# Optimization experiments

Measured on AMD Instinct MI355X. Metric: run time of the kernel, lower is better.

Reference implementation:

```python
import jax, jax.numpy as jnp
import numpy as np

EPS = 1e-5

def _layer_norm(x, gamma, beta):
    mu = jnp.mean(x, axis=-1, keepdims=True)
    var = jnp.mean(jnp.square(x - mu), axis=-1, keepdims=True)
    return (x - mu) * jax.lax.rsqrt(var + EPS) * gamma + beta

def setup_inputs() -> dict:
    key = jax.random.key(0)
    ks = jax.random.split(key, 6)
    B, D, H = 8192, 1024, 1024
    x = jax.random.normal(ks[0], (B, D), dtype=jnp.float32)
    h0 = jax.random.normal(ks[1], (B, H), dtype=jnp.float32)
    c0 = jax.random.normal(ks[2], (B, H), dtype=jnp.float32)
    # learned params (orthogonal init approximated by scaled normal for reference purposes)
    weight_h = jax.random.normal(ks[3], (H, 4 * H), dtype=jnp.float32) / np.sqrt(H)
    weight_x = jax.random.normal(ks[4], (D, 4 * H), dtype=jnp.float32) / np.sqrt(D)
    bias = jnp.zeros((4 * H,), dtype=jnp.float32).at[:H].set(1.0)  # forget-gate bias init to 1
    ln1_g = jnp.ones((4 * H,), jnp.float32); ln1_b = jnp.zeros((4 * H,), jnp.float32)
    ln2_g = jnp.ones((4 * H,), jnp.float32); ln2_b = jnp.zeros((4 * H,), jnp.float32)
    ln3_g = jnp.ones((H,), jnp.float32); ln3_b = jnp.zeros((H,), jnp.float32)
    return {"x": x, "h0": h0, "c0": c0, "weight_h": weight_h, "weight_x": weight_x,
            "bias": bias, "ln1_g": ln1_g, "ln1_b": ln1_b, "ln2_g": ln2_g, "ln2_b": ln2_b,
            "ln3_g": ln3_g, "ln3_b": ln3_b}

def reference(x, h0, c0, weight_h, weight_x, bias, ln1_g, ln1_b, ln2_g, ln2_b, ln3_g, ln3_b):
    # gates: [B, 4H] = LN(h0 @ Wh) + LN(x @ Wx) + bias
    gates = _layer_norm(h0 @ weight_h, ln1_g, ln1_b) + _layer_norm(x @ weight_x, ln2_g, ln2_b) + bias
    H = h0.shape[-1]
    f_g, i_g, o_g, c_g = jnp.split(gates, 4, axis=1)  # forget, in, out, cell
    c1 = jax.nn.sigmoid(f_g) * c0 + jax.nn.sigmoid(i_g) * jnp.tanh(c_g)
    h1 = jax.nn.sigmoid(o_g) * jnp.tanh(_layer_norm(c1, ln3_g, ln3_b))
    return (h1, c1)
```

## Files before the change

kernel.cpp:

```cpp
#include <hip/hip_runtime.h>
#include <cstdint>

#define B_ROWS 8192
#define KDIM 1024
#define N4 4096

typedef __attribute__((ext_vector_type(8))) short short8;
typedef __attribute__((ext_vector_type(4))) float float4v;

__device__ __forceinline__ unsigned short f2bf(float f) {
  union { float f; unsigned int u; } v; v.f = f;
  unsigned int r = v.u + 0x7fffu + ((v.u >> 16) & 1u);
  return (unsigned short)(r >> 16);
}

__device__ __forceinline__ float bf2f(unsigned short s) {
  union { unsigned int u; float f; } v; v.u = ((unsigned int)s) << 16;
  return v.f;
}

__device__ __forceinline__ void async16(const unsigned short* g, unsigned short* l) {
  auto gp = (const __attribute__((address_space(1))) unsigned int*)(uintptr_t)g;
  auto lp = (__attribute__((address_space(3))) unsigned int*)(unsigned int)(uintptr_t)l;
  __builtin_amdgcn_global_load_lds(gp, lp, 16, 0, 0);
}

__device__ __forceinline__ float sigm(float v) { return 1.f / (1.f + expf(-v)); }


__global__ __launch_bounds__(256) void cast_bf16(const float* __restrict__ in0,
                                                 unsigned short* __restrict__ out0,
                                                 const float* __restrict__ in1,
                                                 unsigned short* __restrict__ out1) {
  const float* in = blockIdx.y ? in1 : in0;
  unsigned short* out = blockIdx.y ? out1 : out0;
  int i = (blockIdx.x * 256 + threadIdx.x) * 4;
  float4 v = *(const float4*)(in + i);
  ushort4 o;
  o.x = f2bf(v.x); o.y = f2bf(v.y); o.z = f2bf(v.z); o.w = f2bf(v.w);
  *(ushort4*)(out + i) = o;
}

__global__ __launch_bounds__(256) void transpose_cast(const float* __restrict__ W0,
                                                      unsigned short* __restrict__ Wt0,
                                                      const float* __restrict__ W1,
                                                      unsigned short* __restrict__ Wt1) {
  const float* W = blockIdx.z ? W1 : W0;
  unsigned short* Wt = blockIdx.z ? Wt1 : Wt0;
  __shared__ float tile[32][33];
  int n0 = blockIdx.x * 32;
  int k0 = blockIdx.y * 32;
  int tx = threadIdx.x & 31;
  int ty = threadIdx.x >> 5;
#pragma unroll
  for (int i = 0; i < 32; i += 8)
    tile[ty + i][tx] = W[(size_t)(k0 + ty + i) * N4 + n0 + tx];
  __syncthreads();
#pragma unroll
  for (int i = 0; i < 32; i += 8)
    Wt[(size_t)(n0 + ty + i) * KDIM + k0 + tx] = f2bf(tile[tx][ty + i]);
}


__global__ __launch_bounds__(256) void gemm_bf16(
    const unsigned short* __restrict__ Ah, const unsigned short* __restrict__ Wth,
    unsigned short* __restrict__ Uh,
    const unsigned short* __restrict__ Ax, const unsigned short* __restrict__ Wtx,
    unsigned short* __restrict__ Ux, int row0) {
  const unsigned short* A; const unsigned short* W; unsigned short* U;
  if (blockIdx.z == 0) { A = Ah; W = Wth; U = Uh; } else { A = Ax; W = Wtx; U = Ux; }

  __shared__ unsigned short ldsA[128 * 64];
  __shared__ unsigned short ldsB[128 * 64];

  const int tid = threadIdx.x;
  const int wave = tid >> 6;
  const int lane = tid & 63;
  const int wm = (wave & 1) * 64;
  const int wn = (wave >> 1) * 64;

  const int m0 = row0 + blockIdx.y * 128;
  const int n0 = blockIdx.x * 128;

  const int r8 = lane >> 3;
  const int c8 = lane & 7;
  const int g8 = (c8 - r8) & 7;
  const unsigned short* gA0 = A + (size_t)(m0 + wave * 32 + r8) * KDIM + g8 * 8;
  const unsigned short* gB0 = W + (size_t)(n0 + wave * 32 + r8) * KDIM + g8 * 8;
  unsigned short* lA0 = ldsA + (wave * 32) * 64;
  unsigned short* lB0 = ldsB + (wave * 32) * 64;

  const short8* fA[2][4];
  const short8* fB[2][4];
#pragma unroll
  for (int kh = 0; kh < 2; ++kh)
#pragma unroll
    for (int i = 0; i < 4; ++i) {
      int ma = wm + i * 16 + (lane & 15);
      int qa = kh * 4 + (lane >> 4);
      fA[kh][i] = (const short8*)(ldsA + ma * 64 + (((qa + ma) & 7) * 8));
      int nb = wn + i * 16 + (lane & 15);
      int qb = kh * 4 + (lane >> 4);
      fB[kh][i] = (const short8*)(ldsB + nb * 64 + (((qb + nb) & 7) * 8));
    }

  float4v acc[4][4];
  float4v zero = {0.f, 0.f, 0.f, 0.f};
#pragma unroll
  for (int i = 0; i < 4; ++i)
#pragma unroll
    for (int j = 0; j < 4; ++j) acc[i][j] = zero;

  for (int kt = 0; kt < KDIM; kt += 64) {
#pragma unroll
    for (int j = 0; j < 4; ++j) {
      async16(gA0 + kt + j * 8 * KDIM, lA0 + j * 8 * 64);
      async16(gB0 + kt + j * 8 * KDIM, lB0 + j * 8 * 64);
    }
    __syncthreads();
#pragma unroll
    for (int kh = 0; kh < 2; ++kh) {
      short8 a[4], b[4];
#pragma unroll
      for (int i = 0; i < 4; ++i) { a[i] = *fA[kh][i]; b[i] = *fB[kh][i]; }
#pragma unroll
      for (int mi = 0; mi < 4; ++mi)
#pragma unroll
        for (int ni = 0; ni < 4; ++ni)
          acc[mi][ni] = __builtin_amdgcn_mfma_f32_16x16x32_bf16(a[mi], b[ni], acc[mi][ni], 0, 0, 0);
    }
    __syncthreads();
  }

  const int colc = lane & 15;
  const int rowq = (lane >> 4) * 4;
  unsigned short* Ub = U + (size_t)(blockIdx.y * 128 + wm + rowq) * N4 + n0 + wn + colc;
#pragma unroll
  for (int mi = 0; mi < 4; ++mi)
#pragma unroll
    for (int r = 0; r < 4; ++r) {
      unsigned short* Urow = Ub + (size_t)(mi * 16 + r) * N4;
#pragma unroll
      for (int ni = 0; ni < 4; ++ni) Urow[ni * 16] = f2bf(acc[mi][ni][r]);
    }
}


__global__ __launch_bounds__(256) void fused_ln_lstm(
    const unsigned short* __restrict__ Uh, const unsigned short* __restrict__ Ux,
    const float* __restrict__ c0, const float* __restrict__ bias,
    const float* __restrict__ g1, const float* __restrict__ b1,
    const float* __restrict__ g2, const float* __restrict__ b2,
    const float* __restrict__ g3, const float* __restrict__ b3,
    float* __restrict__ h1o, float* __restrict__ c1o, int row0) {
  const int t = threadIdx.x;
  const int lane = t & 63;
  const int wv = t >> 6;
  const size_t rloc = blockIdx.x;
  const size_t rabs = rloc + (size_t)row0;

  const ushort4* uh = (const ushort4*)(Uh + rloc * N4);
  const ushort4* ux = (const ushort4*)(Ux + rloc * N4);
  float4 cold = ((const float4*)(c0 + rabs * KDIM))[t];

  float4 vh[4], vx[4];
  float sh = 0.f, qh = 0.f, sx = 0.f, qx = 0.f;
#pragma unroll
  for (int k = 0; k < 4; ++k) {
    ushort4 au = uh[k * 256 + t];
    float4 a; a.x = bf2f(au.x); a.y = bf2f(au.y); a.z = bf2f(au.z); a.w = bf2f(au.w);
    vh[k] = a;
    sh += (a.x + a.y) + (a.z + a.w);
    qh += a.x * a.x + a.y * a.y + a.z * a.z + a.w * a.w;
    ushort4 bu = ux[k * 256 + t];
    float4 b; b.x = bf2f(bu.x); b.y = bf2f(bu.y); b.z = bf2f(bu.z); b.w = bf2f(bu.w);
    vx[k] = b;
    sx += (b.x + b.y) + (b.z + b.w);
    qx += b.x * b.x + b.y * b.y + b.z * b.z + b.w * b.w;
  }
  __shared__ float red[4][4];
#pragma unroll
  for (int o = 32; o > 0; o >>= 1) {
    sh += __shfl_down(sh, o); qh += __shfl_down(qh, o);
    sx += __shfl_down(sx, o); qx += __shfl_down(qx, o);
  }
  if (lane == 0) { red[wv][0] = sh; red[wv][1] = qh; red[wv][2] = sx; red[wv][3] = qx; }
  __syncthreads();
  sh = red[0][0] + red[1][0] + red[2][0] + red[3][0];
  qh = red[0][1] + red[1][1] + red[2][1] + red[3][1];
  sx = red[0][2] + red[1][2] + red[2][2] + red[3][2];
  qx = red[0][3] + red[1][3] + red[2][3] + red[3][3];
  const float inv4 = 1.f / 4096.f;
  const float muh = sh * inv4, mux = sx * inv4;
  const float rsh = rsqrtf(qh * inv4 - muh * muh + 1e-5f);
  const float rsx = rsqrtf(qx * inv4 - mux * mux + 1e-5f);

  float4 gate[4];
#pragma unroll
  for (int k = 0; k < 4; ++k) {
    int j = k * 256 + t;
    float4 G1 = ((const float4*)g1)[j], B1 = ((const float4*)b1)[j];
    float4 G2 = ((const float4*)g2)[j], B2 = ((const float4*)b2)[j];
    float4 BB = ((const float4*)bias)[j];
    float4 a = vh[k], b = vx[k], r;
    r.x = (a.x - muh) * rsh * G1.x + B1.x + (b.x - mux) * rsx * G2.x + B2.x + BB.x;
    r.y = (a.y - muh) * rsh * G1.y + B1.y + (b.y - mux) * rsx * G2.y + B2.y + BB.y;
    r.z = (a.z - muh) * rsh * G1.z + B1.z + (b.z - mux) * rsx * G2.z + B2.z + BB.z;
    r.w = (a.w - muh) * rsh * G1.w + B1.w + (b.w - mux) * rsx * G2.w + B2.w + BB.w;
    gate[k] = r;
  }
  float4 fg = gate[0], ig = gate[1], og = gate[2], cg = gate[3];
  float4 c1v;
  c1v.x = sigm(fg.x) * cold.x + sigm(ig.x) * tanhf(cg.x);
  c1v.y = sigm(fg.y) * cold.y + sigm(ig.y) * tanhf(cg.y);
  c1v.z = sigm(fg.z) * cold.z + sigm(ig.z) * tanhf(cg.z);
  c1v.w = sigm(fg.w) * cold.w + sigm(ig.w) * tanhf(cg.w);

  float sc = (c1v.x + c1v.y) + (c1v.z + c1v.w);
  float qc = c1v.x * c1v.x + c1v.y * c1v.y + c1v.z * c1v.z + c1v.w * c1v.w;
#pragma unroll
  for (int o = 32; o > 0; o >>= 1) { sc += __shfl_down(sc, o); qc += __shfl_down(qc, o); }
  __syncthreads();
  if (lane == 0) { red[wv][0] = sc; red[wv][1] = qc; }
  __syncthreads();
  sc = red[0][0] + red[1][0] + red[2][0] + red[3][0];
  qc = red[0][1] + red[1][1] + red[2][1] + red[3][1];
  const float invH = 1.f / 1024.f;
  const float muc = sc * invH;
  const float rsc = rsqrtf(qc * invH - muc * muc + 1e-5f);
  float4 G3 = ((const float4*)g3)[t], B3 = ((const float4*)b3)[t];
  float4 h1v;
  h1v.x = sigm(og.x) * tanhf((c1v.x - muc) * rsc * G3.x + B3.x);
  h1v.y = sigm(og.y) * tanhf((c1v.y - muc) * rsc * G3.y + B3.y);
  h1v.z = sigm(og.z) * tanhf((c1v.z - muc) * rsc * G3.z + B3.z);
  h1v.w = sigm(og.w) * tanhf((c1v.w - muc) * rsc * G3.w + B3.w);

  ((float4*)(h1o + rabs * KDIM))[t] = h1v;
  ((float4*)(c1o + rabs * KDIM))[t] = c1v;
}


extern "C" void kernel_launch(void* const* d_in, const int* in_sizes, int n_in,
                              void* d_out, int out_size, void* d_ws, size_t ws_size,
                              hipStream_t stream) {
  const float* x    = (const float*)d_in[0];
  const float* h0   = (const float*)d_in[1];
  const float* c0   = (const float*)d_in[2];
  const float* Wh   = (const float*)d_in[3];
  const float* Wx   = (const float*)d_in[4];
  const float* bias = (const float*)d_in[5];
  const float* g1   = (const float*)d_in[6];
  const float* b1   = (const float*)d_in[7];
  const float* g2   = (const float*)d_in[8];
  const float* b2   = (const float*)d_in[9];
  const float* g3   = (const float*)d_in[10];
  const float* b3   = (const float*)d_in[11];
  float* h1o = (float*)d_out;
  float* c1o = h1o + (size_t)B_ROWS * KDIM;

  unsigned short* Ah  = (unsigned short*)d_ws;
  unsigned short* Ax  = Ah + (size_t)B_ROWS * KDIM;
  unsigned short* Wth = Ax + (size_t)B_ROWS * KDIM;
  unsigned short* Wtx = Wth + (size_t)N4 * KDIM;
  unsigned short* U = Wtx + (size_t)N4 * KDIM;
  size_t used = ((size_t)B_ROWS * KDIM * 2 + (size_t)N4 * KDIM * 2) * sizeof(unsigned short);
  size_t rem = ws_size > used ? ws_size - used : 0;
  int chunk = (int)(rem / ((size_t)2 * N4 * sizeof(unsigned short)));
  chunk &= ~127;
  if (chunk > B_ROWS) chunk = B_ROWS;
  if (chunk < 128) chunk = 128;

  cast_bf16<<<dim3(B_ROWS * KDIM / 1024, 2), 256, 0, stream>>>(h0, Ah, x, Ax);
  transpose_cast<<<dim3(N4 / 32, KDIM / 32, 2), 256, 0, stream>>>(Wh, Wth, Wx, Wtx);

  for (int r0 = 0; r0 < B_ROWS; r0 += chunk) {
    int rows = chunk;
    if (r0 + rows > B_ROWS) rows = B_ROWS - r0;
    unsigned short* Uh = U;
    unsigned short* Ux = U + (size_t)rows * N4;
    gemm_bf16<<<dim3(N4 / 128, rows / 128, 2), 256, 0, stream>>>(Ah, Wth, Uh, Ax, Wtx, Ux, r0);
    fused_ln_lstm<<<rows, 256, 0, stream>>>(Uh, Ux, c0, bias, g1, b1, g2, b2, g3, b3, h1o, c1o, r0);
  }
}
```

Measured before the change: 373.3 us.

## Double-buffer GEMM LDS, remap blocks per XCD, use fast sigmoid/tanh

The bf16 GEMM now double-buffers LDS tiles and issues the async global-to-LDS loads for the next K step while MFMAs run on the current one. Hand-placed waitcnt/barrier calls and s_setprio bracket the MFMA bursts. Workgroup IDs are remapped so consecutive tiles land on the same XCD for better L2 reuse, and launch bounds now request two blocks per CU. The LSTM epilogue swaps expf/tanhf for hardware exp2/rcp intrinsics, which lowers transcendental cost at some precision risk. LDS use per block doubles, which may limit occupancy.

```diff
diff --git a/kernel.cpp b/kernel.cpp
--- a/kernel.cpp
+++ b/kernel.cpp
@@ -25,7 +25,12 @@
   __builtin_amdgcn_global_load_lds(gp, lp, 16, 0, 0);
 }
 
-__device__ __forceinline__ float sigm(float v) { return 1.f / (1.f + expf(-v)); }
+__device__ __forceinline__ float sigm(float v) {
+  return __builtin_amdgcn_rcpf(1.f + __builtin_amdgcn_exp2f(-1.44269504088896f * v));
+}
+__device__ __forceinline__ float tanh_f(float v) {
+  return 1.f - 2.f * __builtin_amdgcn_rcpf(1.f + __builtin_amdgcn_exp2f(2.88539008177793f * v));
+}
 
 
 __global__ __launch_bounds__(256) void cast_bf16(const float* __restrict__ in0,
@@ -62,7 +67,7 @@
 }
 
 
-__global__ __launch_bounds__(256) void gemm_bf16(
+__global__ __launch_bounds__(256, 2) void gemm_bf16(
     const unsigned short* __restrict__ Ah, const unsigned short* __restrict__ Wth,
     unsigned short* __restrict__ Uh,
     const unsigned short* __restrict__ Ax, const unsigned short* __restrict__ Wtx,
@@ -70,8 +75,8 @@
   const unsigned short* A; const unsigned short* W; unsigned short* U;
   if (blockIdx.z == 0) { A = Ah; W = Wth; U = Uh; } else { A = Ax; W = Wtx; U = Ux; }
 
-  __shared__ unsigned short ldsA[128 * 64];
-  __shared__ unsigned short ldsB[128 * 64];
+  __shared__ unsigned short ldsA[2 * 128 * 64];
+  __shared__ unsigned short ldsB[2 * 128 * 64];
 
   const int tid = threadIdx.x;
   const int wave = tid >> 6;
@@ -79,30 +84,35 @@
   const int wm = (wave & 1) * 64;
   const int wn = (wave >> 1) * 64;
 
-  const int m0 = row0 + blockIdx.y * 128;
-  const int n0 = blockIdx.x * 128;
+  const int gx = N4 / 128;
+  const int nwg = gx * (int)gridDim.y;
+  const int f = (int)blockIdx.y * gx + (int)blockIdx.x;
+  const int qq = nwg >> 3, rr = nwg & 7;
+  const int xcd = f & 7, idx = f >> 3;
+  const int wg = (xcd < rr) ? (xcd * (qq + 1) + idx)
+                            : (rr * (qq + 1) + (xcd - rr) * qq + idx);
+  const int bx = wg & (gx - 1);
+  const int by = wg / gx;
+
+  const int m0 = row0 + by * 128;
+  const int n0 = bx * 128;
 
   const int r8 = lane >> 3;
   const int c8 = lane & 7;
-  const int g8 = (c8 - r8) & 7;
-  const unsigned short* gA0 = A + (size_t)(m0 + wave * 32 + r8) * KDIM + g8 * 8;
-  const unsigned short* gB0 = W + (size_t)(n0 + wave * 32 + r8) * KDIM + g8 * 8;
-  unsigned short* lA0 = ldsA + (wave * 32) * 64;
-  unsigned short* lB0 = ldsB + (wave * 32) * 64;
-
-  const short8* fA[2][4];
-  const short8* fB[2][4];
-#pragma unroll
-  for (int kh = 0; kh < 2; ++kh)
-#pragma unroll
-    for (int i = 0; i < 4; ++i) {
-      int ma = wm + i * 16 + (lane & 15);
-      int qa = kh * 4 + (lane >> 4);
-      fA[kh][i] = (const short8*)(ldsA + ma * 64 + (((qa + ma) & 7) * 8));
-      int nb = wn + i * 16 + (lane & 15);
-      int qb = kh * 4 + (lane >> 4);
-      fB[kh][i] = (const short8*)(ldsB + nb * 64 + (((qb + nb) & 7) * 8));
-    }
+  const int g8 = ((c8 - r8) & 7) * 8;
+  const int aR = wave * 32;
+  const int beR = (wave & 1) * 16 + (wave >> 1) * 64;
+  const int blR = beR + 32;
+
+  const unsigned short* gA  = A + (size_t)(m0 + aR + r8) * KDIM + g8;
+  const unsigned short* gBe = W + (size_t)(n0 + beR + r8) * KDIM + g8;
+  const unsigned short* gBl = W + (size_t)(n0 + blR + r8) * KDIM + g8;
+
+  const int lq = lane & 15, lh = lane >> 4;
+  const int offA0 = (wm + lq) * 64 + ((lh + lq) & 7) * 8;
+  const int offA1 = (wm + lq) * 64 + ((4 + lh + lq) & 7) * 8;
+  const int offB0 = (wn + lq) * 64 + ((lh + lq) & 7) * 8;
+  const int offB1 = (wn + lq) * 64 + ((4 + lh + lq) & 7) * 8;
 
   float4v acc[4][4];
   float4v zero = {0.f, 0.f, 0.f, 0.f};
@@ -111,37 +121,79 @@
 #pragma unroll
     for (int j = 0; j < 4; ++j) acc[i][j] = zero;
 
-  for (int kt = 0; kt < KDIM; kt += 64) {
-#pragma unroll
-    for (int j = 0; j < 4; ++j) {
-      async16(gA0 + kt + j * 8 * KDIM, lA0 + j * 8 * 64);
-      async16(gB0 + kt + j * 8 * KDIM, lB0 + j * 8 * 64);
+#pragma unroll
+  for (int j = 0; j < 4; ++j) async16(gA + j * 8 * KDIM, ldsA + (aR + j * 8) * 64);
+  async16(gBe, ldsB + beR * 64);
+  async16(gBe + 8 * KDIM, ldsB + (beR + 8) * 64);
+  async16(gBl, ldsB + blR * 64);
+  async16(gBl + 8 * KDIM, ldsB + (blR + 8) * 64);
+  asm volatile("s_waitcnt vmcnt(2)\n\ts_barrier" ::: "memory");
+
+  short8 aF[4][2], bF[2][2];
+
+#pragma unroll 2
+  for (int t = 0; t < KDIM / 64; ++t) {
+    const unsigned short* sA = ldsA + (t & 1) * 8192;
+    const unsigned short* sB = ldsB + (t & 1) * 8192;
+    unsigned short* nA = (unsigned short*)ldsA + ((t + 1) & 1) * 8192;
+    unsigned short* nB = (unsigned short*)ldsB + ((t + 1) & 1) * 8192;
+    const int kNX = (t + 1) * 64;
+
+#pragma unroll
+    for (int mi = 0; mi < 4; ++mi) {
+      aF[mi][0] = *(const short8*)(sA + offA0 + mi * 1024);
+      aF[mi][1] = *(const short8*)(sA + offA1 + mi * 1024);
     }
-    __syncthreads();
-#pragma unroll
-    for (int kh = 0; kh < 2; ++kh) {
-      short8 a[4], b[4];
-#pragma unroll
-      for (int i = 0; i < 4; ++i) { a[i] = *fA[kh][i]; b[i] = *fB[kh][i]; }
+#pragma unroll
+    for (int nj = 0; nj < 2; ++nj) {
+      bF[nj][0] = *(const short8*)(sB + offB0 + nj * 1024);
+      bF[nj][1] = *(const short8*)(sB + offB1 + nj * 1024);
+    }
+#pragma unroll
+    for (int j = 0; j < 4; ++j) async16(gA + kNX + j * 8 * KDIM, nA + (aR + j * 8) * 64);
+    async16(gBe + kNX, nB + beR * 64);
+    async16(gBe + kNX + 8 * KDIM, nB + (beR + 8) * 64);
+    __builtin_amdgcn_s_setprio(1);
+#pragma unroll
+    for (int kh = 0; kh < 2; ++kh)
 #pragma unroll
       for (int mi = 0; mi < 4; ++mi)
 #pragma unroll
-        for (int ni = 0; ni < 4; ++ni)
-          acc[mi][ni] = __builtin_amdgcn_mfma_f32_16x16x32_bf16(a[mi], b[ni], acc[mi][ni], 0, 0, 0);
+        for (int nj = 0; nj < 2; ++nj)
+          acc[mi][nj] = __builtin_amdgcn_mfma_f32_16x16x32_bf16(aF[mi][kh], bF[nj][kh], acc[mi][nj], 0, 0, 0);
+    __builtin_amdgcn_s_setprio(0);
+    asm volatile("s_waitcnt vmcnt(6)\n\ts_barrier" ::: "memory");
+
+#pragma unroll
+    for (int nj = 0; nj < 2; ++nj) {
+      bF[nj][0] = *(const short8*)(sB + offB0 + (2 + nj) * 1024);
+      bF[nj][1] = *(const short8*)(sB + offB1 + (2 + nj) * 1024);
     }
-    __syncthreads();
-  }
+    async16(gBl + kNX, nB + blR * 64);
+    async16(gBl + kNX + 8 * KDIM, nB + (blR + 8) * 64);
+    __builtin_amdgcn_s_setprio(1);
+#pragma unroll
+    for (int kh = 0; kh < 2; ++kh)
+#pragma unroll
+      for (int mi = 0; mi < 4; ++mi)
+#pragma unroll
+        for (int nj = 0; nj < 2; ++nj)
+          acc[mi][2 + nj] = __builtin_amdgcn_mfma_f32_16x16x32_bf16(aF[mi][kh], bF[nj][kh], acc[mi][2 + nj], 0, 0, 0);
+    __builtin_amdgcn_s_setprio(0);
+    asm volatile("s_waitcnt vmcnt(2)\n\ts_barrier" ::: "memory");
+  }
+  asm volatile("s_waitcnt vmcnt(0)" ::: "memory");
 
   const int colc = lane & 15;
   const int rowq = (lane >> 4) * 4;
-  unsigned short* Ub = U + (size_t)(blockIdx.y * 128 + wm + rowq) * N4 + n0 + wn + colc;
+  unsigned short* Ub = U + (size_t)(by * 128 + wm + rowq) * N4 + n0 + wn + colc;
 #pragma unroll
   for (int mi = 0; mi < 4; ++mi)
 #pragma unroll
     for (int r = 0; r < 4; ++r) {
       unsigned short* Urow = Ub + (size_t)(mi * 16 + r) * N4;
 #pragma unroll
-      for (int ni = 0; ni < 4; ++ni) Urow[ni * 16] = f2bf(acc[mi][ni][r]);
+      for (int nj = 0; nj < 4; ++nj) Urow[nj * 16] = f2bf(acc[mi][nj][r]);
     }
 }
 
@@ -211,10 +263,10 @@
   }
   float4 fg = gate[0], ig = gate[1], og = gate[2], cg = gate[3];
   float4 c1v;
-  c1v.x = sigm(fg.x) * cold.x + sigm(ig.x) * tanhf(cg.x);
-  c1v.y = sigm(fg.y) * cold.y + sigm(ig.y) * tanhf(cg.y);
-  c1v.z = sigm(fg.z) * cold.z + sigm(ig.z) * tanhf(cg.z);
-  c1v.w = sigm(fg.w) * cold.w + sigm(ig.w) * tanhf(cg.w);
+  c1v.x = sigm(fg.x) * cold.x + sigm(ig.x) * tanh_f(cg.x);
+  c1v.y = sigm(fg.y) * cold.y + sigm(ig.y) * tanh_f(cg.y);
+  c1v.z = sigm(fg.z) * cold.z + sigm(ig.z) * tanh_f(cg.z);
+  c1v.w = sigm(fg.w) * cold.w + sigm(ig.w) * tanh_f(cg.w);
 
   float sc = (c1v.x + c1v.y) + (c1v.z + c1v.w);
   float qc = c1v.x * c1v.x + c1v.y * c1v.y + c1v.z * c1v.z + c1v.w * c1v.w;
@@ -230,10 +282,10 @@
   const float rsc = rsqrtf(qc * invH - muc * muc + 1e-5f);
   float4 G3 = ((const float4*)g3)[t], B3 = ((const float4*)b3)[t];
   float4 h1v;
-  h1v.x = sigm(og.x) * tanhf((c1v.x - muc) * rsc * G3.x + B3.x);
-  h1v.y = sigm(og.y) * tanhf((c1v.y - muc) * rsc * G3.y + B3.y);
-  h1v.z = sigm(og.z) * tanhf((c1v.z - muc) * rsc * G3.z + B3.z);
-  h1v.w = sigm(og.w) * tanhf((c1v.w - muc) * rsc * G3.w + B3.w);
+  h1v.x = sigm(og.x) * tanh_f((c1v.x - muc) * rsc * G3.x + B3.x);
+  h1v.y = sigm(og.y) * tanh_f((c1v.y - muc) * rsc * G3.y + B3.y);
+  h1v.z = sigm(og.z) * tanh_f((c1v.z - muc) * rsc * G3.z + B3.z);
+  h1v.w = sigm(og.w) * tanh_f((c1v.w - muc) * rsc * G3.w + B3.w);
 
   ((float4*)(h1o + rabs * KDIM))[t] = h1v;
   ((float4*)(c1o + rabs * KDIM))[t] = c1v;
```

After: 389.8 us. 1.04x slower.
